# Performance work log

Measured on AMD Instinct MI355X. Metric: run time of the kernel, lower is better.

## Reference

```python
import jax, jax.numpy as jnp
import numpy as np
from jax import lax

K_NEIGHBORS = 15
LAM = 1.0
EPS = 1e-8


def _cdist(a):
    # Euclidean pairwise distance, safe sqrt (zero diag has zero grad path handled in bwd module too)
    sq = jnp.sum(a * a, axis=1)
    d2 = sq[:, None] + sq[None, :] - 2.0 * (a @ a.T)
    d2 = jnp.maximum(d2, 0.0)
    safe = jnp.where(d2 > 0.0, d2, 1.0)
    return jnp.where(d2 > 0.0, jnp.sqrt(safe), 0.0)


def _knn_loss(z, x, k):
    B = x.shape[0]
    x_dist = _cdist(x)
    z_dist = _cdist(z)
    eye = jnp.eye(B, dtype=bool)
    x_ns = jnp.where(eye, jnp.inf, x_dist)  # fill_diagonal_(inf)
    _, knn_idx = lax.top_k(-x_ns, k)        # k smallest per row
    mask = jnp.zeros((B, B), dtype=bool).at[jnp.arange(B)[:, None], knn_idx].set(True)
    mask = mask | mask.T
    x_max = jnp.max(jnp.where(mask, x_dist, -jnp.inf))
    z_max = jnp.max(jnp.where(mask, z_dist, -jnp.inf))
    x_norm = x_dist / (x_max + EPS)
    z_norm = z_dist / (z_max + EPS)
    diff2 = (z_norm - x_norm) ** 2
    # mean over masked entries == masked_select(...).mean()
    return jnp.sum(jnp.where(mask, diff2, 0.0)) / jnp.sum(mask).astype(diff2.dtype)


def setup_inputs() -> dict:
    key = jax.random.key(0)
    ks = jax.random.split(key, 13)
    D, H1, H2, L = 1024, 2048, 512, 64

    def lin(k, fan_in, fan_out):
        bound = 1.0 / np.sqrt(fan_in)
        kw, kb = jax.random.split(k)
        w = jax.random.uniform(kw, (fan_in, fan_out), jnp.float32, -bound, bound)
        b = jax.random.uniform(kb, (fan_out,), jnp.float32, -bound, bound)
        return w, b

    x = jax.random.normal(ks[0], (8192, D), jnp.float32)
    w_e0, b_e0 = lin(ks[1], D, H1)
    w_e1, b_e1 = lin(ks[2], H1, H2)
    w_e2, b_e2 = lin(ks[3], H2, L)
    w_d0, b_d0 = lin(ks[4], L, H2)
    w_d1, b_d1 = lin(ks[5], H2, H1)
    w_d2, b_d2 = lin(ks[6], H1, D)
    return {"x": x,
            "w_e0": w_e0, "b_e0": b_e0, "w_e1": w_e1, "b_e1": b_e1, "w_e2": w_e2, "b_e2": b_e2,
            "w_d0": w_d0, "b_d0": b_d0, "w_d1": w_d1, "b_d1": b_d1, "w_d2": w_d2, "b_d2": b_d2}


def reference(x, w_e0, b_e0, w_e1, b_e1, w_e2, b_e2, w_d0, b_d0, w_d1, b_d1, w_d2, b_d2):
    h = jax.nn.relu(x @ w_e0 + b_e0)
    h = jax.nn.relu(h @ w_e1 + b_e1)
    z = h @ w_e2 + b_e2
    h = jax.nn.relu(z @ w_d0 + b_d0)
    h = jax.nn.relu(h @ w_d1 + b_d1)
    x_rec = h @ w_d2 + b_d2
    rec_loss = jnp.mean((x_rec - x) ** 2)
    knn_loss = _knn_loss(z, x, K_NEIGHBORS)
    total = rec_loss + LAM * knn_loss
    return (total, z, rec_loss, knn_loss)
```

## Files before the change

### kernel.cpp

```cpp
#include <hip/hip_runtime.h>


typedef __attribute__((ext_vector_type(8))) short bf16x8;
typedef __attribute__((ext_vector_type(4))) float f32x4;

#define DEVINL static __device__ __forceinline__

DEVINL unsigned short f2bf(float f){
  unsigned u = __float_as_uint(f);
  u += 0x7FFFu + ((u >> 16) & 1u);
  return (unsigned short)(u >> 16);
}

DEVINL int med3i(int a, int b, int c){
  int d;
  asm("v_med3_i32 %0, %1, %2, %3" : "=v"(d) : "v"(a), "v"(b), "v"(c));
  return d;
}

DEVINL void gload16(const unsigned short* g, void* lds){
  __builtin_amdgcn_global_load_lds(
      (const __attribute__((address_space(1))) unsigned int*)g,
      (__attribute__((address_space(3))) unsigned int*)lds, 16, 0, 0);
}

DEVINL void lds_barrier(){
  asm volatile("s_waitcnt lgkmcnt(0)" ::: "memory");
  __builtin_amdgcn_s_barrier();
  asm volatile("" ::: "memory");
}

#define NLISTS 47

__global__ __launch_bounds__(256) void cvt_rowsq_k(const float* __restrict__ x,
    unsigned short* __restrict__ xb, float* __restrict__ xsq){
  const int lane = threadIdx.x & 63, wv = threadIdx.x >> 6;
  const int row = blockIdx.x * 4 + wv;
  const float4* px = (const float4*)(x + (size_t)row * 1024);
  ushort4* pb = (ushort4*)(xb + (size_t)row * 1024);
  float ss = 0.f;
  #pragma unroll
  for (int q = 0; q < 4; q++){
    float4 v = px[q * 64 + lane];
    ss += v.x*v.x + v.y*v.y + v.z*v.z + v.w*v.w;
    ushort4 o; o.x = f2bf(v.x); o.y = f2bf(v.y); o.z = f2bf(v.z); o.w = f2bf(v.w);
    pb[q * 64 + lane] = o;
  }
  #pragma unroll
  for (int o = 32; o; o >>= 1) ss += __shfl_xor(ss, o);
  if (!lane) xsq[row] = ss;
}

template<int BM, int BN, int WM, int WN, bool RELU, int OMODE>
__global__ __launch_bounds__(256, 2) void gemm_bt(
    const unsigned short* __restrict__ A, const unsigned short* __restrict__ Bt,
    const float* __restrict__ bias, int M, int N, int K,
    unsigned short* __restrict__ Cb, float* __restrict__ Cf,
    const float* __restrict__ Xref, float* __restrict__ recPart)
{
  constexpr int FM = BM / (WM * 16), FN = BN / (WN * 16);
  __shared__ short As[BM][32];
  __shared__ short Bs[BN][32];
  __shared__ float wsum[4];
  const int tid = threadIdx.x, lane = tid & 63, wid = tid >> 6;
  const int wr = wid / WN, wc = wid % WN;
  const int r16 = lane & 15, kg = lane >> 4;
  const int row0 = blockIdx.x * BM, col0 = blockIdx.y * BN;
  const int srow = lane >> 2, scol = (lane & 3) * 8;
  (void)M;
  f32x4 acc[FM][FN] = {};
  for (int k0 = 0; k0 < K; k0 += 32){
    __syncthreads();
    for (int ch = wid; ch < BM/16; ch += 4)
      gload16(A + (size_t)(row0 + ch*16 + srow) * K + k0 + scol, &As[ch*16][0]);
    for (int ch = wid; ch < BN/16; ch += 4)
      gload16(Bt + (size_t)(col0 + ch*16 + srow) * K + k0 + scol, &Bs[ch*16][0]);
    __syncthreads();
    bf16x8 af[FM], bfr[FN];
    #pragma unroll
    for (int m = 0; m < FM; m++) af[m]  = *(const bf16x8*)&As[wr*FM*16 + m*16 + r16][kg*8];
    #pragma unroll
    for (int n = 0; n < FN; n++) bfr[n] = *(const bf16x8*)&Bs[wc*FN*16 + n*16 + r16][kg*8];
    #pragma unroll
    for (int m = 0; m < FM; m++)
      #pragma unroll
      for (int n = 0; n < FN; n++)
        acc[m][n] = __builtin_amdgcn_mfma_f32_16x16x32_bf16(af[m], bfr[n], acc[m][n], 0, 0, 0);
  }
  float lsum = 0.f;
  #pragma unroll
  for (int m = 0; m < FM; m++){
    #pragma unroll
    for (int n = 0; n < FN; n++){
      const int gc = col0 + wc*FN*16 + n*16 + r16;
      const float bv = bias[gc];
      #pragma unroll
      for (int r = 0; r < 4; r++){
        const int gr = row0 + wr*FM*16 + m*16 + kg*4 + r;
        float v = acc[m][n][r] + bv;
        if (RELU) v = fmaxf(v, 0.f);
        if (OMODE == 2){
          float d = v - Xref[(size_t)gr * N + gc];
          lsum += d * d;
        } else {
          Cb[(size_t)gr * N + gc] = f2bf(v);
          if (OMODE == 1) Cf[(size_t)gr * N + gc] = v;
        }
      }
    }
  }
  if (OMODE == 2){
    #pragma unroll
    for (int o = 32; o; o >>= 1) lsum += __shfl_xor(lsum, o);
    if (!lane) wsum[wid] = lsum;
    __syncthreads();
    if (!tid) recPart[blockIdx.y * gridDim.x + blockIdx.x] =
        wsum[0] + wsum[1] + wsum[2] + wsum[3];
  }
}

__global__ __launch_bounds__(256, 2) void gram_topk_k(
    const unsigned short* __restrict__ Xb, const float* __restrict__ xsq,
    int* __restrict__ topP,
    const float* __restrict__ w0, const float* __restrict__ w1,
    const float* __restrict__ w2, const float* __restrict__ w3,
    const float* __restrict__ w4, const float* __restrict__ w5,
    unsigned short* __restrict__ t0, unsigned short* __restrict__ t1,
    unsigned short* __restrict__ t2, unsigned short* __restrict__ t3,
    unsigned short* __restrict__ t4, unsigned short* __restrict__ t5)
{
  __shared__ short As[128][32];
  __shared__ short Bs[128][32];
  __shared__ unsigned short d2s[128][130];
  __shared__ int colL[128][15];
  const int tid = threadIdx.x, lane = tid & 63, wid = tid >> 6;

  if (blockIdx.x >= 512){
    int id = blockIdx.x - 512;
    const float* w; unsigned short* wt; int K, N, loc;
    if      (id < 2048){ w = w0; wt = t0; K = 1024; N = 2048; loc = id; }
    else if (id < 3072){ w = w1; wt = t1; K = 2048; N = 512;  loc = id - 2048; }
    else if (id < 3104){ w = w2; wt = t2; K = 512;  N = 64;   loc = id - 3072; }
    else if (id < 3136){ w = w3; wt = t3; K = 64;   N = 512;  loc = id - 3104; }
    else if (id < 4160){ w = w4; wt = t4; K = 512;  N = 2048; loc = id - 3136; }
    else               { w = w5; wt = t5; K = 2048; N = 1024; loc = id - 4160; }
    const int ntn = N >> 5;
    const int n0 = (loc % ntn) << 5, k0 = (loc / ntn) << 5;
    float (*t)[33] = (float (*)[33])As;
    const int tx = tid & 31, ty = tid >> 5;
    #pragma unroll
    for (int q = 0; q < 4; q++)
      t[ty + 8*q][tx] = w[(size_t)(k0 + ty + 8*q) * N + n0 + tx];
    __syncthreads();
    #pragma unroll
    for (int q = 0; q < 4; q++)
      wt[(size_t)(n0 + ty + 8*q) * K + k0 + tx] = f2bf(t[tx][ty + 8*q]);
    return;
  }

  const int wr = wid >> 1, wc = wid & 1;
  const int r16 = lane & 15, kg = lane >> 4;
  const int srow = lane >> 2, scol = (lane & 3) * 8;
  const float INF = __builtin_inff();
  const int INFI = 0x7FFFFFFF;

  const int bi = blockIdx.x & 63;
  const int cl = blockIdx.x >> 6;
  const int row0 = bi * 128;
  const int ntt = (cl == 7) ? 5 : 4;

  const int selrow = tid & 127, half = tid >> 7, selc0 = half * 64;

  auto stage = [&](int j0s, int k0s){
    for (int ch = wid; ch < 8; ch += 4){
      gload16(Xb + (size_t)(row0 + ch*16 + srow) * 1024 + k0s + scol, &As[ch*16][0]);
      gload16(Xb + (size_t)(j0s  + ch*16 + srow) * 1024 + k0s + scol, &Bs[ch*16][0]);
    }
  };

  int r0,r1,r2,r3,r4,r5,r6,r7,r8,r9,r10,r11,r12,r13,r14;
  r0=r1=r2=r3=r4=r5=r6=r7=r8=r9=r10=r11=r12=r13=r14=INFI;
  auto insR = [&](int v){
    if (v < r14){
      r14 = med3i(v, r13, r14); r13 = med3i(v, r12, r13);
      r12 = med3i(v, r11, r12); r11 = med3i(v, r10, r11);
      r10 = med3i(v, r9 , r10); r9  = med3i(v, r8 , r9 );
      r8  = med3i(v, r7 , r8 ); r7  = med3i(v, r6 , r7 );
      r6  = med3i(v, r5 , r6 ); r5  = med3i(v, r4 , r5 );
      r4  = med3i(v, r3 , r4 ); r3  = med3i(v, r2 , r3 );
      r2  = med3i(v, r1 , r2 ); r1  = med3i(v, r0 , r1 );
      r0  = min(r0, v);
    }
  };
  int c0,c1,c2,c3,c4,c5,c6,c7,c8,c9,c10,c11,c12,c13,c14;
  auto insC = [&](int v){
    if (v < c14){
      c14 = med3i(v, c13, c14); c13 = med3i(v, c12, c13);
      c12 = med3i(v, c11, c12); c11 = med3i(v, c10, c11);
      c10 = med3i(v, c9 , c10); c9  = med3i(v, c8 , c9 );
      c8  = med3i(v, c7 , c8 ); c7  = med3i(v, c6 , c7 );
      c6  = med3i(v, c5 , c6 ); c5  = med3i(v, c4 , c5 );
      c4  = med3i(v, c3 , c4 ); c3  = med3i(v, c2 , c3 );
      c2  = med3i(v, c1 , c2 ); c1  = med3i(v, c0 , c1 );
      c0  = min(c0, v);
    }
  };

  float xr[4][4];
  #pragma unroll
  for (int m = 0; m < 4; m++)
    #pragma unroll
    for (int r = 0; r < 4; r++)
      xr[m][r] = xsq[row0 + wr*64 + m*16 + kg*4 + r];

  stage(((bi + cl * 4) & 63) * 128, 0);

  for (int tt = 0; tt < ntt; ++tt){
    const int d = cl * 4 + tt;
    const int bj = (bi + d) & 63;
    const int j0 = bj * 128;
    f32x4 acc[4][4] = {};
    for (int k0 = 0; k0 < 1024; k0 += 32){
      __syncthreads();
      bf16x8 af[4], bfr[4];
      #pragma unroll
      for (int m = 0; m < 4; m++) af[m]  = *(const bf16x8*)&As[wr*64 + m*16 + r16][kg*8];
      #pragma unroll
      for (int n = 0; n < 4; n++) bfr[n] = *(const bf16x8*)&Bs[wc*64 + n*16 + r16][kg*8];
      __syncthreads();
      if (k0 + 32 < 1024)      stage(j0, k0 + 32);
      else if (tt + 1 < ntt)   stage(((bi + d + 1) & 63) * 128, 0);
      #pragma unroll
      for (int m = 0; m < 4; m++)
        #pragma unroll
        for (int n = 0; n < 4; n++)
          acc[m][n] = __builtin_amdgcn_mfma_f32_16x16x32_bf16(af[m], bfr[n], acc[m][n], 0, 0, 0);
    }
    float xc[4];
    #pragma unroll
    for (int n = 0; n < 4; n++) xc[n] = xsq[j0 + wc*64 + n*16 + r16];
    #pragma unroll
    for (int m = 0; m < 4; m++){
      #pragma unroll
      for (int n = 0; n < 4; n++){
        const int lc = wc*64 + n*16 + r16;
        #pragma unroll
        for (int r = 0; r < 4; r++){
          const int lr = wr*64 + m*16 + kg*4 + r;
          float v = xr[m][r] + xc[n] - 2.f * acc[m][n][r];
          if (row0 + lr == j0 + lc) v = INF;
          d2s[lr][lc] = f2bf(v);
        }
      }
    }
    lds_barrier();
    const int jg0 = j0 + selc0;
    #pragma unroll 4
    for (int cc = 0; cc < 64; cc += 2){
      unsigned pv = *(const unsigned*)&d2s[selrow][selc0 + cc];
      insR((int)(((pv & 0xFFFFu) << 16) | (unsigned)(jg0 + cc)));
      insR((int)((pv & 0xFFFF0000u) | (unsigned)(jg0 + cc + 1)));
    }
    const bool doCol = (d >= 1) && (d <= 31);
    if (doCol){
      c0=c1=c2=c3=c4=c5=c6=c7=c8=c9=c10=c11=c12=c13=c14=INFI;
      const int rbase = row0 + selc0;
      #pragma unroll 4
      for (int rr = 0; rr < 64; ++rr){
        unsigned v = d2s[selc0 + rr][selrow];
        insC((int)((v << 16) | (unsigned)(rbase + rr)));
      }
      if (half){
        colL[selrow][0]=c0;  colL[selrow][1]=c1;  colL[selrow][2]=c2;
        colL[selrow][3]=c3;  colL[selrow][4]=c4;  colL[selrow][5]=c5;
        colL[selrow][6]=c6;  colL[selrow][7]=c7;  colL[selrow][8]=c8;
        colL[selrow][9]=c9;  colL[selrow][10]=c10; colL[selrow][11]=c11;
        colL[selrow][12]=c12; colL[selrow][13]=c13; colL[selrow][14]=c14;
      }
    }
    lds_barrier();
    if (doCol && !half){
      #pragma unroll 1
      for (int q = 0; q < 15; ++q){
        int v = colL[selrow][q];
        if (v >= c14) break;
        insC(v);
      }
      int* dst = topP + ((size_t)(j0 + selrow) * NLISTS + (16 + d - 1)) * 15;
      dst[0]=c0;  dst[1]=c1;  dst[2]=c2;  dst[3]=c3;  dst[4]=c4;
      dst[5]=c5;  dst[6]=c6;  dst[7]=c7;  dst[8]=c8;  dst[9]=c9;
      dst[10]=c10; dst[11]=c11; dst[12]=c12; dst[13]=c13; dst[14]=c14;
    }
  }
  int* dst = topP + ((size_t)(row0 + selrow) * NLISTS + (2 * cl + half)) * 15;
  dst[0]=r0;  dst[1]=r1;  dst[2]=r2;  dst[3]=r3;  dst[4]=r4;
  dst[5]=r5;  dst[6]=r6;  dst[7]=r7;  dst[8]=r8;  dst[9]=r9;
  dst[10]=r10; dst[11]=r11; dst[12]=r12; dst[13]=r13; dst[14]=r14;
}

__global__ __launch_bounds__(256) void merge_topk_k(const int* __restrict__ topP,
    int* __restrict__ knn, float* __restrict__ d2k, float* __restrict__ xpart)
{
  __shared__ float wmax[4];
  const int lane = threadIdx.x & 63, wid = threadIdx.x >> 6;
  const int row = blockIdx.x * 4 + wid;
  const int* tp = topP + (size_t)row * (NLISTS * 15);
  const int INFI = 0x7FFFFFFF;
  int c0  = tp[lane];
  int c1  = tp[lane + 64];
  int c2  = tp[lane + 128];
  int c3  = tp[lane + 192];
  int c4  = tp[lane + 256];
  int c5  = tp[lane + 320];
  int c6  = tp[lane + 384];
  int c7  = tp[lane + 448];
  int c8  = tp[lane + 512];
  int c9  = tp[lane + 576];
  int c10 = tp[lane + 640];
  int c11 = (lane + 704 < 705) ? tp[lane + 704] : INFI;
  float last = 0.f;
  for (int it = 0; it < 15; ++it){
    int m = min(min(min(c0, c1), min(c2, c3)), min(min(c4, c5), min(c6, c7)));
    m = min(m, min(min(c8, c9), min(c10, c11)));
    #pragma unroll
    for (int o = 32; o; o >>= 1) m = min(m, __shfl_xor(m, o));
    if (!lane){
      knn[row * 15 + it] = m & 0xFFFF;
      float f = __uint_as_float((unsigned)m & 0xFFFF0000u);
      d2k[row * 15 + it] = f;
      last = f;
    }
    c0  = (c0  == m) ? INFI : c0;   c1  = (c1  == m) ? INFI : c1;
    c2  = (c2  == m) ? INFI : c2;   c3  = (c3  == m) ? INFI : c3;
    c4  = (c4  == m) ? INFI : c4;   c5  = (c5  == m) ? INFI : c5;
    c6  = (c6  == m) ? INFI : c6;   c7  = (c7  == m) ? INFI : c7;
    c8  = (c8  == m) ? INFI : c8;   c9  = (c9  == m) ? INFI : c9;
    c10 = (c10 == m) ? INFI : c10;  c11 = (c11 == m) ? INFI : c11;
  }
  if (!lane) wmax[wid] = last;
  __syncthreads();
  if (!threadIdx.x)
    xpart[blockIdx.x] = fmaxf(fmaxf(wmax[0], wmax[1]), fmaxf(wmax[2], wmax[3]));
}

__global__ void mask_build_k(const int* __restrict__ knn, unsigned* __restrict__ mask){
  int t = blockIdx.x * blockDim.x + threadIdx.x;
  if (t >= 8192 * 15) return;
  int i = t / 15, j = knn[t];
  atomicOr(&mask[i * 256 + (j >> 5)], 1u << (j & 31));
  atomicOr(&mask[j * 256 + (i >> 5)], 1u << (i & 31));
}

__global__ __launch_bounds__(256) void rowcnt_k(const unsigned* __restrict__ mask,
                                                int* __restrict__ rowcnt){
  const int lane = threadIdx.x & 63, wid = threadIdx.x >> 6;
  const int row = blockIdx.x * 4 + wid;
  const unsigned* mr = mask + (size_t)row * 256;
  int pc = __popc(mr[lane]) + __popc(mr[64+lane]) + __popc(mr[128+lane]) + __popc(mr[192+lane]);
  #pragma unroll
  for (int o = 32; o; o >>= 1) pc += __shfl_xor(pc, o);
  if (!lane) rowcnt[row] = pc;
}

__global__ __launch_bounds__(1024) void scan_k(const int* __restrict__ rowcnt,
                                               int* __restrict__ rowbase, int* __restrict__ count){
  __shared__ int sc[1024];
  const int t = threadIdx.x;
  int local[8];
  int s = 0;
  #pragma unroll
  for (int q = 0; q < 8; q++){ local[q] = s; s += rowcnt[t * 8 + q]; }
  sc[t] = s;
  __syncthreads();
  for (int o = 1; o < 1024; o <<= 1){
    int v = (t >= o) ? sc[t - o] : 0;
    __syncthreads();
    sc[t] += v;
    __syncthreads();
  }
  const int base = t ? sc[t - 1] : 0;
  #pragma unroll
  for (int q = 0; q < 8; q++) rowbase[t * 8 + q] = base + local[q];
  if (t == 1023) count[0] = sc[1023];
}

__global__ __launch_bounds__(256) void gather2_k(const unsigned* __restrict__ mask,
                                                 const int* __restrict__ rowbase,
                                                 unsigned* __restrict__ pairs){
  const int lane = threadIdx.x & 63, wid = threadIdx.x >> 6;
  const int row = blockIdx.x * 4 + wid;
  const unsigned* mr = mask + (size_t)row * 256;
  unsigned w0 = mr[lane], w1 = mr[64+lane], w2 = mr[128+lane], w3 = mr[192+lane];
  const int pc = __popc(w0) + __popc(w1) + __popc(w2) + __popc(w3);
  int s = pc;
  for (int o = 1; o < 64; o <<= 1){
    int v = __shfl_up(s, o);
    if (lane >= o) s += v;
  }
  int base = rowbase[row] + s - pc;
  const unsigned hi = (unsigned)row << 16;
  unsigned w; int jb;
  w = w0; jb = lane * 32;
  while (w){ int b = __ffs(w) - 1; w &= w - 1; pairs[base++] = hi | (unsigned)(jb + b); }
  w = w1; jb = (64 + lane) * 32;
  while (w){ int b = __ffs(w) - 1; w &= w - 1; pairs[base++] = hi | (unsigned)(jb + b); }
  w = w2; jb = (128 + lane) * 32;
  while (w){ int b = __ffs(w) - 1; w &= w - 1; pairs[base++] = hi | (unsigned)(jb + b); }
  w = w3; jb = (192 + lane) * 32;
  while (w){ int b = __ffs(w) - 1; w &= w - 1; pairs[base++] = hi | (unsigned)(jb + b); }
}

__global__ __launch_bounds__(256) void pair_sums_k(
    const unsigned* __restrict__ pairs, const int* __restrict__ count,
    const float* __restrict__ z, const int* __restrict__ knn, const float* __restrict__ d2k,
    float* __restrict__ zzP, float* __restrict__ zxP, float* __restrict__ xxP,
    float* __restrict__ zmP)
{
  __shared__ float red[4][4];
  const int lane = threadIdx.x & 63, wid = threadIdx.x >> 6;
  const int n = *count;
  float szz = 0.f, szx = 0.f, sxx = 0.f, mz = 0.f;
  for (int p = blockIdx.x * 4 + wid; p < n; p += gridDim.x * 4){
    const unsigned pr = pairs[p];
    const int i = (int)(pr >> 16), j = (int)(pr & 0xFFFFu);
    float d = z[i * 64 + lane] - z[j * 64 + lane];
    float s = d * d;
    #pragma unroll
    for (int o = 32; o; o >>= 1) s += __shfl_xor(s, o);
    int ki = knn[i * 15 + min(lane, 14)];
    unsigned long long m1 = __ballot(lane < 15 && ki == j);
    float dx2;
    if (m1){
      dx2 = d2k[i * 15 + (__ffsll(m1) - 1)];
    } else {
      int kj = knn[j * 15 + min(lane, 14)];
      unsigned long long m2 = __ballot(lane < 15 && kj == i);
      dx2 = d2k[j * 15 + (__ffsll(m2) - 1)];
    }
    float dz = sqrtf(s), dx = sqrtf(dx2);
    szz += s;
    szx += dz * dx;
    sxx += dx2;
    mz = fmaxf(mz, dz);
  }
  if (!lane){ red[wid][0] = szz; red[wid][1] = szx; red[wid][2] = sxx; red[wid][3] = mz; }
  __syncthreads();
  if (!threadIdx.x){
    float a = 0.f, b = 0.f, c = 0.f, m = 0.f;
    #pragma unroll
    for (int w = 0; w < 4; w++){
      a += red[w][0]; b += red[w][1]; c += red[w][2]; m = fmaxf(m, red[w][3]);
    }
    zzP[blockIdx.x] = a; zxP[blockIdx.x] = b; xxP[blockIdx.x] = c; zmP[blockIdx.x] = m;
  }
}

__global__ __launch_bounds__(256) void final_reduce_k(
    const float* __restrict__ recPart, const float* __restrict__ xpart,
    const float* __restrict__ zzP, const float* __restrict__ zxP,
    const float* __restrict__ xxP, const float* __restrict__ zmP,
    const int* __restrict__ count, float* __restrict__ out)
{
  __shared__ float rd[4][6];
  const int t = threadIdx.x, lane = t & 63, wid = t >> 6;
  float rec = 0.f, xm = 0.f, zz = 0.f, zx = 0.f, xx = 0.f, zm = 0.f;
  for (int i = t; i < 1024; i += 256) rec += recPart[i];
  for (int i = t; i < 2048; i += 256) xm = fmaxf(xm, xpart[i]);
  for (int i = t; i < 1920; i += 256){
    zz += zzP[i]; zx += zxP[i]; xx += xxP[i]; zm = fmaxf(zm, zmP[i]);
  }
  #pragma unroll
  for (int o = 32; o; o >>= 1){
    rec += __shfl_xor(rec, o); zz += __shfl_xor(zz, o);
    zx  += __shfl_xor(zx, o);  xx += __shfl_xor(xx, o);
    xm = fmaxf(xm, __shfl_xor(xm, o));
    zm = fmaxf(zm, __shfl_xor(zm, o));
  }
  if (!lane){
    rd[wid][0]=rec; rd[wid][1]=zz; rd[wid][2]=zx; rd[wid][3]=xx; rd[wid][4]=xm; rd[wid][5]=zm;
  }
  __syncthreads();
  if (!t){
    rec = rd[0][0]+rd[1][0]+rd[2][0]+rd[3][0];
    zz  = rd[0][1]+rd[1][1]+rd[2][1]+rd[3][1];
    zx  = rd[0][2]+rd[1][2]+rd[2][2]+rd[3][2];
    xx  = rd[0][3]+rd[1][3]+rd[2][3]+rd[3][3];
    xm  = fmaxf(fmaxf(rd[0][4],rd[1][4]), fmaxf(rd[2][4],rd[3][4]));
    zm  = fmaxf(fmaxf(rd[0][5],rd[1][5]), fmaxf(rd[2][5],rd[3][5]));
    rec *= 1.0f / (8192.0f * 1024.0f);
    float xmax = sqrtf(xm);
    float rx = 1.0f / (xmax + 1e-8f), rz = 1.0f / (zm + 1e-8f);
    float knn = (zz * rz * rz - 2.0f * zx * rz * rx + xx * rx * rx) / (float)count[0];
    out[0] = rec + knn;
    out[1 + 8192 * 64]     = rec;
    out[1 + 8192 * 64 + 1] = knn;
  }
}

extern "C" void kernel_launch(void* const* d_in, const int* in_sizes, int n_in,
                              void* d_out, int out_size, void* d_ws, size_t ws_size,
                              hipStream_t stream)
{
  (void)in_sizes; (void)n_in; (void)out_size;
  const float* x    = (const float*)d_in[0];
  const float* w_e0 = (const float*)d_in[1];  const float* b_e0 = (const float*)d_in[2];
  const float* w_e1 = (const float*)d_in[3];  const float* b_e1 = (const float*)d_in[4];
  const float* w_e2 = (const float*)d_in[5];  const float* b_e2 = (const float*)d_in[6];
  const float* w_d0 = (const float*)d_in[7];  const float* b_d0 = (const float*)d_in[8];
  const float* w_d1 = (const float*)d_in[9];  const float* b_d1 = (const float*)d_in[10];
  const float* w_d2 = (const float*)d_in[11]; const float* b_d2 = (const float*)d_in[12];
  float* out = (float*)d_out;

  char* ws = (char*)d_ws;
  size_t off = 0;
  auto alloc = [&](size_t bytes) -> void* {
    void* p = ws + off;
    off += (bytes + 255) & ~(size_t)255;
    return p;
  };
  unsigned short* xb   = (unsigned short*)alloc(8192ull * 1024 * 2);
  unsigned short* wte0 = (unsigned short*)alloc(2048ull * 1024 * 2);
  unsigned short* wte1 = (unsigned short*)alloc(512ull  * 2048 * 2);
  unsigned short* wte2 = (unsigned short*)alloc(64ull   * 512  * 2);
  unsigned short* wtd0 = (unsigned short*)alloc(512ull  * 64   * 2);
  unsigned short* wtd1 = (unsigned short*)alloc(2048ull * 512  * 2);
  unsigned short* wtd2 = (unsigned short*)alloc(1024ull * 2048 * 2);
  unsigned short* bufA = (unsigned short*)alloc(8192ull * 2048 * 2);
  unsigned short* bufB = (unsigned short*)alloc(8192ull * 512  * 2);
  unsigned short* zb   = (unsigned short*)alloc(8192ull * 64   * 2);
  float* xsq    = (float*)alloc(8192 * 4);
  int*   knn    = (int*)  alloc(8192ull * 15 * 4);
  float* d2k    = (float*)alloc(8192ull * 15 * 4);
  unsigned* mask = (unsigned*)alloc(8192ull * 256 * 4);
  int*   rowcnt = (int*)  alloc(8192 * 4);
  int*   rowbase= (int*)  alloc(8192 * 4);
  unsigned* pairs = (unsigned*)alloc(245760ull * 4);
  float* xpart  = (float*)alloc(2048 * 4);
  float* zzP    = (float*)alloc(1920 * 4);
  float* zxP    = (float*)alloc(1920 * 4);
  float* xxP    = (float*)alloc(1920 * 4);
  float* zmP    = (float*)alloc(1920 * 4);
  float* recPart= (float*)alloc(1024 * 4);
  int*   count  = (int*)  alloc(256);
  if (off > ws_size) return;

  int* topP = (int*)bufA;

  hipMemsetAsync(mask, 0, 8192ull * 256 * 4, stream);

  cvt_rowsq_k<<<2048, 256, 0, stream>>>(x, xb, xsq);

  gram_topk_k<<<6720, 256, 0, stream>>>(xb, xsq, topP,
      w_e0, w_e1, w_e2, w_d0, w_d1, w_d2, wte0, wte1, wte2, wtd0, wtd1, wtd2);
  merge_topk_k<<<2048, 256, 0, stream>>>(topP, knn, d2k, xpart);
  mask_build_k<<<(8192 * 15 + 255) / 256, 256, 0, stream>>>(knn, mask);
  rowcnt_k<<<2048, 256, 0, stream>>>(mask, rowcnt);
  scan_k<<<1, 1024, 0, stream>>>(rowcnt, rowbase, count);
  gather2_k<<<2048, 256, 0, stream>>>(mask, rowbase, pairs);

  gemm_bt<128,128,2,2,true ,0><<<dim3(64,16), 256, 0, stream>>>(xb,   wte0, b_e0, 8192, 2048, 1024, bufA, nullptr, nullptr, nullptr);
  gemm_bt<128, 64,2,2,true ,0><<<dim3(64, 8), 256, 0, stream>>>(bufA, wte1, b_e1, 8192,  512, 2048, bufB, nullptr, nullptr, nullptr);
  gemm_bt< 32, 64,2,2,false,1><<<dim3(256,1), 256, 0, stream>>>(bufB, wte2, b_e2, 8192,   64,  512, zb,   out + 1, nullptr, nullptr);
  gemm_bt<128, 64,2,2,true ,0><<<dim3(64, 8), 256, 0, stream>>>(zb,   wtd0, b_d0, 8192,  512,   64, bufB, nullptr, nullptr, nullptr);
  gemm_bt<128,128,2,2,true ,0><<<dim3(64,16), 256, 0, stream>>>(bufB, wtd1, b_d1, 8192, 2048,  512, bufA, nullptr, nullptr, nullptr);
  gemm_bt< 64,128,2,2,false,2><<<dim3(128,8), 256, 0, stream>>>(bufA, wtd2, b_d2, 8192, 1024, 2048, nullptr, nullptr, x, recPart);

  pair_sums_k<<<1920, 256, 0, stream>>>(pairs, count, out + 1, knn, d2k, zzP, zxP, xxP, zmP);
  final_reduce_k<<<1, 256, 0, stream>>>(recPart, xpart, zzP, zxP, xxP, zmP, count, out);
}
```

Baseline: 434.3 us.

## Prefilter kNN candidates with diagonal-block threshold, drop mask pipeline, fuse layer-0 GEMM

Adds a pass that computes a per-row 15th-smallest distance bound from each row's own 128-row diagonal block. The gram/top-k kernel uses this bound to reject most candidates before the med3 insertion network, buffering survivors in LDS, and merges the two half-row lists in-block so fewer partial lists are written. The weight transpose moves into the conversion kernel, and the first encoder GEMM runs as extra blocks inside the gram kernel so the two overlap. The bitmask build, row count, scan and gather kernels are replaced by iterating over kNN pairs directly, weighting each pair by whether it is mutual. This cuts launch count and global traffic, but adds the threshold kernel and puts a heavier mix of work into one kernel.

```diff
diff --git a/kernel.cpp b/kernel.cpp
--- a/kernel.cpp
+++ b/kernel.cpp
@@ -30,11 +30,55 @@
   asm volatile("" ::: "memory");
 }
 
-#define NLISTS 47
-
-__global__ __launch_bounds__(256) void cvt_rowsq_k(const float* __restrict__ x,
-    unsigned short* __restrict__ xb, float* __restrict__ xsq){
-  const int lane = threadIdx.x & 63, wv = threadIdx.x >> 6;
+#define NLISTS 39
+
+#define INS15(NAME, R0,R1,R2,R3,R4,R5,R6,R7,R8,R9,R10,R11,R12,R13,R14)  \
+  auto NAME = [&](int v){                                               \
+    if (v < R14){                                                       \
+      R14 = med3i(v, R13, R14); R13 = med3i(v, R12, R13);               \
+      R12 = med3i(v, R11, R12); R11 = med3i(v, R10, R11);               \
+      R10 = med3i(v, R9 , R10); R9  = med3i(v, R8 , R9 );               \
+      R8  = med3i(v, R7 , R8 ); R7  = med3i(v, R6 , R7 );               \
+      R6  = med3i(v, R5 , R6 ); R5  = med3i(v, R4 , R5 );               \
+      R4  = med3i(v, R3 , R4 ); R3  = med3i(v, R2 , R3 );               \
+      R2  = med3i(v, R1 , R2 ); R1  = med3i(v, R0 , R1 );               \
+      R0  = min(R0, v);                                                 \
+    }                                                                   \
+  }
+
+__global__ __launch_bounds__(256) void cvtT_k(const float* __restrict__ x,
+    unsigned short* __restrict__ xb, float* __restrict__ xsq,
+    const float* __restrict__ w0, const float* __restrict__ w1,
+    const float* __restrict__ w2, const float* __restrict__ w3,
+    const float* __restrict__ w4, const float* __restrict__ w5,
+    unsigned short* __restrict__ t0, unsigned short* __restrict__ t1,
+    unsigned short* __restrict__ t2, unsigned short* __restrict__ t3,
+    unsigned short* __restrict__ t4, unsigned short* __restrict__ t5)
+{
+  __shared__ float t[32][33];
+  const int tid = threadIdx.x;
+  if (blockIdx.x >= 2048){
+    int id = blockIdx.x - 2048;
+    const float* w; unsigned short* wt; int K, N, loc;
+    if      (id < 2048){ w = w0; wt = t0; K = 1024; N = 2048; loc = id; }
+    else if (id < 3072){ w = w1; wt = t1; K = 2048; N = 512;  loc = id - 2048; }
+    else if (id < 3104){ w = w2; wt = t2; K = 512;  N = 64;   loc = id - 3072; }
+    else if (id < 3136){ w = w3; wt = t3; K = 64;   N = 512;  loc = id - 3104; }
+    else if (id < 4160){ w = w4; wt = t4; K = 512;  N = 2048; loc = id - 3136; }
+    else               { w = w5; wt = t5; K = 2048; N = 1024; loc = id - 4160; }
+    const int ntn = N >> 5;
+    const int n0 = (loc % ntn) << 5, k0 = (loc / ntn) << 5;
+    const int tx = tid & 31, ty = tid >> 5;
+    #pragma unroll
+    for (int q = 0; q < 4; q++)
+      t[ty + 8*q][tx] = w[(size_t)(k0 + ty + 8*q) * N + n0 + tx];
+    __syncthreads();
+    #pragma unroll
+    for (int q = 0; q < 4; q++)
+      wt[(size_t)(n0 + ty + 8*q) * K + k0 + tx] = f2bf(t[tx][ty + 8*q]);
+    return;
+  }
+  const int lane = tid & 63, wv = tid >> 6;
   const int row = blockIdx.x * 4 + wv;
   const float4* px = (const float4*)(x + (size_t)row * 1024);
   ushort4* pb = (ushort4*)(xb + (size_t)row * 1024);
@@ -49,6 +93,75 @@
   #pragma unroll
   for (int o = 32; o; o >>= 1) ss += __shfl_xor(ss, o);
   if (!lane) xsq[row] = ss;
+}
+
+__global__ __launch_bounds__(256, 2) void thr_k(
+    const unsigned short* __restrict__ Xb, const float* __restrict__ xsq,
+    int* __restrict__ thrI)
+{
+  __shared__ short As[128][32];
+  __shared__ unsigned short d2s[128][130];
+  const int tid = threadIdx.x, lane = tid & 63, wid = tid >> 6;
+  const int wr = wid >> 1, wc = wid & 1;
+  const int r16 = lane & 15, kg = lane >> 4;
+  const int srow = lane >> 2, scol = (lane & 3) * 8;
+  const float INF = __builtin_inff();
+  const int b0 = blockIdx.x * 128;
+
+  float xr[4][4];
+  #pragma unroll
+  for (int m = 0; m < 4; m++)
+    #pragma unroll
+    for (int r = 0; r < 4; r++)
+      xr[m][r] = xsq[b0 + wr*64 + m*16 + kg*4 + r];
+
+  f32x4 acc[4][4] = {};
+  for (int k0 = 0; k0 < 1024; k0 += 32){
+    __syncthreads();
+    for (int ch = wid; ch < 8; ch += 4)
+      gload16(Xb + (size_t)(b0 + ch*16 + srow) * 1024 + k0 + scol, &As[ch*16][0]);
+    __syncthreads();
+    bf16x8 af[4], bfr[4];
+    #pragma unroll
+    for (int m = 0; m < 4; m++) af[m]  = *(const bf16x8*)&As[wr*64 + m*16 + r16][kg*8];
+    #pragma unroll
+    for (int n = 0; n < 4; n++) bfr[n] = *(const bf16x8*)&As[wc*64 + n*16 + r16][kg*8];
+    #pragma unroll
+    for (int m = 0; m < 4; m++)
+      #pragma unroll
+      for (int n = 0; n < 4; n++)
+        acc[m][n] = __builtin_amdgcn_mfma_f32_16x16x32_bf16(af[m], bfr[n], acc[m][n], 0, 0, 0);
+  }
+  float xc[4];
+  #pragma unroll
+  for (int n = 0; n < 4; n++) xc[n] = xsq[b0 + wc*64 + n*16 + r16];
+  #pragma unroll
+  for (int m = 0; m < 4; m++){
+    #pragma unroll
+    for (int n = 0; n < 4; n++){
+      const int lc = wc*64 + n*16 + r16;
+      #pragma unroll
+      for (int r = 0; r < 4; r++){
+        const int lr = wr*64 + m*16 + kg*4 + r;
+        float v = xr[m][r] + xc[n] - 2.f * acc[m][n][r];
+        if (lr == lc) v = INF;
+        d2s[lr][lc] = f2bf(v);
+      }
+    }
+  }
+  __syncthreads();
+  if (tid < 128){
+    int r0,r1,r2,r3,r4,r5,r6,r7,r8,r9,r10,r11,r12,r13,r14;
+    r0=r1=r2=r3=r4=r5=r6=r7=r8=r9=r10=r11=r12=r13=r14=0x7FFFFFFF;
+    INS15(ins, r0,r1,r2,r3,r4,r5,r6,r7,r8,r9,r10,r11,r12,r13,r14);
+    #pragma unroll 4
+    for (int cc = 0; cc < 128; cc += 2){
+      unsigned pv = *(const unsigned*)&d2s[tid][cc];
+      ins((int)((pv << 16) | (unsigned)cc));
+      ins((int)((pv & 0xFFFF0000u) | (unsigned)(cc + 1)));
+    }
+    thrI[b0 + tid] = (int)(((unsigned)r14 & 0xFFFF0000u) | 0xFFFFu);
+  }
 }
 
 template<int BM, int BN, int WM, int WN, bool RELU, int OMODE>
@@ -121,55 +234,66 @@
 
 __global__ __launch_bounds__(256, 2) void gram_topk_k(
     const unsigned short* __restrict__ Xb, const float* __restrict__ xsq,
-    int* __restrict__ topP,
-    const float* __restrict__ w0, const float* __restrict__ w1,
-    const float* __restrict__ w2, const float* __restrict__ w3,
-    const float* __restrict__ w4, const float* __restrict__ w5,
-    unsigned short* __restrict__ t0, unsigned short* __restrict__ t1,
-    unsigned short* __restrict__ t2, unsigned short* __restrict__ t3,
-    unsigned short* __restrict__ t4, unsigned short* __restrict__ t5)
+    const int* __restrict__ thrI, int* __restrict__ topP,
+    const unsigned short* __restrict__ gBt, const float* __restrict__ gBias,
+    unsigned short* __restrict__ gC)
 {
   __shared__ short As[128][32];
   __shared__ short Bs[128][32];
   __shared__ unsigned short d2s[128][130];
   __shared__ int colL[128][15];
+  __shared__ unsigned bkt[16][256];
   const int tid = threadIdx.x, lane = tid & 63, wid = tid >> 6;
-
-  if (blockIdx.x >= 512){
-    int id = blockIdx.x - 512;
-    const float* w; unsigned short* wt; int K, N, loc;
-    if      (id < 2048){ w = w0; wt = t0; K = 1024; N = 2048; loc = id; }
-    else if (id < 3072){ w = w1; wt = t1; K = 2048; N = 512;  loc = id - 2048; }
-    else if (id < 3104){ w = w2; wt = t2; K = 512;  N = 64;   loc = id - 3072; }
-    else if (id < 3136){ w = w3; wt = t3; K = 64;   N = 512;  loc = id - 3104; }
-    else if (id < 4160){ w = w4; wt = t4; K = 512;  N = 2048; loc = id - 3136; }
-    else               { w = w5; wt = t5; K = 2048; N = 1024; loc = id - 4160; }
-    const int ntn = N >> 5;
-    const int n0 = (loc % ntn) << 5, k0 = (loc / ntn) << 5;
-    float (*t)[33] = (float (*)[33])As;
-    const int tx = tid & 31, ty = tid >> 5;
-    #pragma unroll
-    for (int q = 0; q < 4; q++)
-      t[ty + 8*q][tx] = w[(size_t)(k0 + ty + 8*q) * N + n0 + tx];
-    __syncthreads();
-    #pragma unroll
-    for (int q = 0; q < 4; q++)
-      wt[(size_t)(n0 + ty + 8*q) * K + k0 + tx] = f2bf(t[tx][ty + 8*q]);
-    return;
-  }
-
   const int wr = wid >> 1, wc = wid & 1;
   const int r16 = lane & 15, kg = lane >> 4;
   const int srow = lane >> 2, scol = (lane & 3) * 8;
+
+  if (blockIdx.x >= 512){
+    const int gb = blockIdx.x - 512;
+    const int row0 = (gb & 63) * 128, col0 = (gb >> 6) * 128;
+    f32x4 acc[4][4] = {};
+    for (int k0 = 0; k0 < 1024; k0 += 32){
+      __syncthreads();
+      for (int ch = wid; ch < 8; ch += 4){
+        gload16(Xb  + (size_t)(row0 + ch*16 + srow) * 1024 + k0 + scol, &As[ch*16][0]);
+        gload16(gBt + (size_t)(col0 + ch*16 + srow) * 1024 + k0 + scol, &Bs[ch*16][0]);
+      }
+      __syncthreads();
+      bf16x8 af[4], bfr[4];
+      #pragma unroll
+      for (int m = 0; m < 4; m++) af[m]  = *(const bf16x8*)&As[wr*64 + m*16 + r16][kg*8];
+      #pragma unroll
+      for (int n = 0; n < 4; n++) bfr[n] = *(const bf16x8*)&Bs[wc*64 + n*16 + r16][kg*8];
+      #pragma unroll
+      for (int m = 0; m < 4; m++)
+        #pragma unroll
+        for (int n = 0; n < 4; n++)
+          acc[m][n] = __builtin_amdgcn_mfma_f32_16x16x32_bf16(af[m], bfr[n], acc[m][n], 0, 0, 0);
+    }
+    #pragma unroll
+    for (int m = 0; m < 4; m++){
+      #pragma unroll
+      for (int n = 0; n < 4; n++){
+        const int gc = col0 + wc*64 + n*16 + r16;
+        const float bv = gBias[gc];
+        #pragma unroll
+        for (int r = 0; r < 4; r++){
+          const int gr = row0 + wr*64 + m*16 + kg*4 + r;
+          gC[(size_t)gr * 2048 + gc] = f2bf(fmaxf(acc[m][n][r] + bv, 0.f));
+        }
+      }
+    }
+    return;
+  }
+
   const float INF = __builtin_inff();
   const int INFI = 0x7FFFFFFF;
-
   const int bi = blockIdx.x & 63;
   const int cl = blockIdx.x >> 6;
   const int row0 = bi * 128;
   const int ntt = (cl == 7) ? 5 : 4;
-
   const int selrow = tid & 127, half = tid >> 7, selc0 = half * 64;
+  const int thrRI = thrI[row0 + selrow];
 
   auto stage = [&](int j0s, int k0s){
     for (int ch = wid; ch < 8; ch += 4){
@@ -180,31 +304,9 @@
 
   int r0,r1,r2,r3,r4,r5,r6,r7,r8,r9,r10,r11,r12,r13,r14;
   r0=r1=r2=r3=r4=r5=r6=r7=r8=r9=r10=r11=r12=r13=r14=INFI;
-  auto insR = [&](int v){
-    if (v < r14){
-      r14 = med3i(v, r13, r14); r13 = med3i(v, r12, r13);
-      r12 = med3i(v, r11, r12); r11 = med3i(v, r10, r11);
-      r10 = med3i(v, r9 , r10); r9  = med3i(v, r8 , r9 );
-      r8  = med3i(v, r7 , r8 ); r7  = med3i(v, r6 , r7 );
-      r6  = med3i(v, r5 , r6 ); r5  = med3i(v, r4 , r5 );
-      r4  = med3i(v, r3 , r4 ); r3  = med3i(v, r2 , r3 );
-      r2  = med3i(v, r1 , r2 ); r1  = med3i(v, r0 , r1 );
-      r0  = min(r0, v);
-    }
-  };
+  INS15(insR, r0,r1,r2,r3,r4,r5,r6,r7,r8,r9,r10,r11,r12,r13,r14);
   int c0,c1,c2,c3,c4,c5,c6,c7,c8,c9,c10,c11,c12,c13,c14;
-  auto insC = [&](int v){
-    if (v < c14){
-      c14 = med3i(v, c13, c14); c13 = med3i(v, c12, c13);
-      c12 = med3i(v, c11, c12); c11 = med3i(v, c10, c11);
-      c10 = med3i(v, c9 , c10); c9  = med3i(v, c8 , c9 );
-      c8  = med3i(v, c7 , c8 ); c7  = med3i(v, c6 , c7 );
-      c6  = med3i(v, c5 , c6 ); c5  = med3i(v, c4 , c5 );
-      c4  = med3i(v, c3 , c4 ); c3  = med3i(v, c2 , c3 );
-      c2  = med3i(v, c1 , c2 ); c1  = med3i(v, c0 , c1 );
-      c0  = min(c0, v);
-    }
-  };
+  INS15(insC, c0,c1,c2,c3,c4,c5,c6,c7,c8,c9,c10,c11,c12,c13,c14);
 
   float xr[4][4];
   #pragma unroll
@@ -254,22 +356,40 @@
       }
     }
     lds_barrier();
-    const int jg0 = j0 + selc0;
-    #pragma unroll 4
-    for (int cc = 0; cc < 64; cc += 2){
-      unsigned pv = *(const unsigned*)&d2s[selrow][selc0 + cc];
-      insR((int)(((pv & 0xFFFFu) << 16) | (unsigned)(jg0 + cc)));
-      insR((int)((pv & 0xFFFF0000u) | (unsigned)(jg0 + cc + 1)));
-    }
+
+    {
+      int cnt = 0;
+      const int jg0 = j0 + selc0;
+      #pragma unroll 4
+      for (int cc = 0; cc < 64; cc += 2){
+        unsigned pv = *(const unsigned*)&d2s[selrow][selc0 + cc];
+        int p0 = (int)((pv << 16) | (unsigned)(jg0 + cc));
+        int p1 = (int)((pv & 0xFFFF0000u) | (unsigned)(jg0 + cc + 1));
+        if (p0 <= thrRI){
+          if (cnt < 16){ bkt[cnt][tid] = (unsigned)p0; ++cnt; } else insR(p0);
+        }
+        if (p1 <= thrRI){
+          if (cnt < 16){ bkt[cnt][tid] = (unsigned)p1; ++cnt; } else insR(p1);
+        }
+      }
+      for (int q = 0; q < cnt; ++q) insR((int)bkt[q][tid]);
+    }
+
     const bool doCol = (d >= 1) && (d <= 31);
     if (doCol){
       c0=c1=c2=c3=c4=c5=c6=c7=c8=c9=c10=c11=c12=c13=c14=INFI;
+      const int thrCI = thrI[j0 + selrow];
       const int rbase = row0 + selc0;
+      int cnt = 0;
       #pragma unroll 4
       for (int rr = 0; rr < 64; ++rr){
         unsigned v = d2s[selc0 + rr][selrow];
-        insC((int)((v << 16) | (unsigned)(rbase + rr)));
-      }
+        int pk = (int)((v << 16) | (unsigned)(rbase + rr));
+        if (pk <= thrCI){
+          if (cnt < 16){ bkt[cnt][tid] = (unsigned)pk; ++cnt; } else insC(pk);
+        }
+      }
+      for (int q = 0; q < cnt; ++q) insC((int)bkt[q][tid]);
       if (half){
         colL[selrow][0]=c0;  colL[selrow][1]=c1;  colL[selrow][2]=c2;
         colL[selrow][3]=c3;  colL[selrow][4]=c4;  colL[selrow][5]=c5;
@@ -286,16 +406,33 @@
         if (v >= c14) break;
         insC(v);
       }
-      int* dst = topP + ((size_t)(j0 + selrow) * NLISTS + (16 + d - 1)) * 15;
+      int* dst = topP + ((size_t)(j0 + selrow) * NLISTS + (8 + d - 1)) * 15;
       dst[0]=c0;  dst[1]=c1;  dst[2]=c2;  dst[3]=c3;  dst[4]=c4;
       dst[5]=c5;  dst[6]=c6;  dst[7]=c7;  dst[8]=c8;  dst[9]=c9;
       dst[10]=c10; dst[11]=c11; dst[12]=c12; dst[13]=c13; dst[14]=c14;
     }
   }
-  int* dst = topP + ((size_t)(row0 + selrow) * NLISTS + (2 * cl + half)) * 15;
-  dst[0]=r0;  dst[1]=r1;  dst[2]=r2;  dst[3]=r3;  dst[4]=r4;
-  dst[5]=r5;  dst[6]=r6;  dst[7]=r7;  dst[8]=r8;  dst[9]=r9;
-  dst[10]=r10; dst[11]=r11; dst[12]=r12; dst[13]=r13; dst[14]=r14;
+  lds_barrier();
+  if (half){
+    colL[selrow][0]=r0;  colL[selrow][1]=r1;  colL[selrow][2]=r2;
+    colL[selrow][3]=r3;  colL[selrow][4]=r4;  colL[selrow][5]=r5;
+    colL[selrow][6]=r6;  colL[selrow][7]=r7;  colL[selrow][8]=r8;
+    colL[selrow][9]=r9;  colL[selrow][10]=r10; colL[selrow][11]=r11;
+    colL[selrow][12]=r12; colL[selrow][13]=r13; colL[selrow][14]=r14;
+  }
+  lds_barrier();
+  if (!half){
+    #pragma unroll 1
+    for (int q = 0; q < 15; ++q){
+      int v = colL[selrow][q];
+      if (v >= r14) break;
+      insR(v);
+    }
+    int* dst = topP + ((size_t)(row0 + selrow) * NLISTS + cl) * 15;
+    dst[0]=r0;  dst[1]=r1;  dst[2]=r2;  dst[3]=r3;  dst[4]=r4;
+    dst[5]=r5;  dst[6]=r6;  dst[7]=r7;  dst[8]=r8;  dst[9]=r9;
+    dst[10]=r10; dst[11]=r11; dst[12]=r12; dst[13]=r13; dst[14]=r14;
+  }
 }
 
 __global__ __launch_bounds__(256) void merge_topk_k(const int* __restrict__ topP,
@@ -306,22 +443,20 @@
   const int row = blockIdx.x * 4 + wid;
   const int* tp = topP + (size_t)row * (NLISTS * 15);
   const int INFI = 0x7FFFFFFF;
-  int c0  = tp[lane];
-  int c1  = tp[lane + 64];
-  int c2  = tp[lane + 128];
-  int c3  = tp[lane + 192];
-  int c4  = tp[lane + 256];
-  int c5  = tp[lane + 320];
-  int c6  = tp[lane + 384];
-  int c7  = tp[lane + 448];
-  int c8  = tp[lane + 512];
-  int c9  = tp[lane + 576];
-  int c10 = tp[lane + 640];
-  int c11 = (lane + 704 < 705) ? tp[lane + 704] : INFI;
+  int c0 = tp[lane];
+  int c1 = tp[lane + 64];
+  int c2 = tp[lane + 128];
+  int c3 = tp[lane + 192];
+  int c4 = tp[lane + 256];
+  int c5 = tp[lane + 320];
+  int c6 = tp[lane + 384];
+  int c7 = tp[lane + 448];
+  int c8 = tp[lane + 512];
+  int c9 = (lane < 9) ? tp[lane + 576] : INFI;
   float last = 0.f;
   for (int it = 0; it < 15; ++it){
     int m = min(min(min(c0, c1), min(c2, c3)), min(min(c4, c5), min(c6, c7)));
-    m = min(m, min(min(c8, c9), min(c10, c11)));
+    m = min(m, min(c8, c9));
     #pragma unroll
     for (int o = 32; o; o >>= 1) m = min(m, __shfl_xor(m, o));
     if (!lane){
@@ -330,12 +465,11 @@
       d2k[row * 15 + it] = f;
       last = f;
     }
-    c0  = (c0  == m) ? INFI : c0;   c1  = (c1  == m) ? INFI : c1;
-    c2  = (c2  == m) ? INFI : c2;   c3  = (c3  == m) ? INFI : c3;
-    c4  = (c4  == m) ? INFI : c4;   c5  = (c5  == m) ? INFI : c5;
-    c6  = (c6  == m) ? INFI : c6;   c7  = (c7  == m) ? INFI : c7;
-    c8  = (c8  == m) ? INFI : c8;   c9  = (c9  == m) ? INFI : c9;
-    c10 = (c10 == m) ? INFI : c10;  c11 = (c11 == m) ? INFI : c11;
+    c0 = (c0 == m) ? INFI : c0;   c1 = (c1 == m) ? INFI : c1;
+    c2 = (c2 == m) ? INFI : c2;   c3 = (c3 == m) ? INFI : c3;
+    c4 = (c4 == m) ? INFI : c4;   c5 = (c5 == m) ? INFI : c5;
+    c6 = (c6 == m) ? INFI : c6;   c7 = (c7 == m) ? INFI : c7;
+    c8 = (c8 == m) ? INFI : c8;   c9 = (c9 == m) ? INFI : c9;
   }
   if (!lane) wmax[wid] = last;
   __syncthreads();
@@ -343,115 +477,47 @@
     xpart[blockIdx.x] = fmaxf(fmaxf(wmax[0], wmax[1]), fmaxf(wmax[2], wmax[3]));
 }
 
-__global__ void mask_build_k(const int* __restrict__ knn, unsigned* __restrict__ mask){
-  int t = blockIdx.x * blockDim.x + threadIdx.x;
-  if (t >= 8192 * 15) return;
-  int i = t / 15, j = knn[t];
-  atomicOr(&mask[i * 256 + (j >> 5)], 1u << (j & 31));
-  atomicOr(&mask[j * 256 + (i >> 5)], 1u << (i & 31));
-}
-
-__global__ __launch_bounds__(256) void rowcnt_k(const unsigned* __restrict__ mask,
-                                                int* __restrict__ rowcnt){
+__global__ __launch_bounds__(256) void pair_sums_k(
+    const float* __restrict__ z, const int* __restrict__ knn,
+    const float* __restrict__ d2k,
+    float* __restrict__ zzP, float* __restrict__ zxP, float* __restrict__ xxP,
+    float* __restrict__ zmP, float* __restrict__ cntP)
+{
+  __shared__ float red[4][5];
   const int lane = threadIdx.x & 63, wid = threadIdx.x >> 6;
-  const int row = blockIdx.x * 4 + wid;
-  const unsigned* mr = mask + (size_t)row * 256;
-  int pc = __popc(mr[lane]) + __popc(mr[64+lane]) + __popc(mr[128+lane]) + __popc(mr[192+lane]);
-  #pragma unroll
-  for (int o = 32; o; o >>= 1) pc += __shfl_xor(pc, o);
-  if (!lane) rowcnt[row] = pc;
-}
-
-__global__ __launch_bounds__(1024) void scan_k(const int* __restrict__ rowcnt,
-                                               int* __restrict__ rowbase, int* __restrict__ count){
-  __shared__ int sc[1024];
-  const int t = threadIdx.x;
-  int local[8];
-  int s = 0;
-  #pragma unroll
-  for (int q = 0; q < 8; q++){ local[q] = s; s += rowcnt[t * 8 + q]; }
-  sc[t] = s;
-  __syncthreads();
-  for (int o = 1; o < 1024; o <<= 1){
-    int v = (t >= o) ? sc[t - o] : 0;
-    __syncthreads();
-    sc[t] += v;
-    __syncthreads();
-  }
-  const int base = t ? sc[t - 1] : 0;
-  #pragma unroll
-  for (int q = 0; q < 8; q++) rowbase[t * 8 + q] = base + local[q];
-  if (t == 1023) count[0] = sc[1023];
-}
-
-__global__ __launch_bounds__(256) void gather2_k(const unsigned* __restrict__ mask,
-                                                 const int* __restrict__ rowbase,
-                                                 unsigned* __restrict__ pairs){
-  const int lane = threadIdx.x & 63, wid = threadIdx.x >> 6;
-  const int row = blockIdx.x * 4 + wid;
-  const unsigned* mr = mask + (size_t)row * 256;
-  unsigned w0 = mr[lane], w1 = mr[64+lane], w2 = mr[128+lane], w3 = mr[192+lane];
-  const int pc = __popc(w0) + __popc(w1) + __popc(w2) + __popc(w3);
-  int s = pc;
-  for (int o = 1; o < 64; o <<= 1){
-    int v = __shfl_up(s, o);
-    if (lane >= o) s += v;
-  }
-  int base = rowbase[row] + s - pc;
-  const unsigned hi = (unsigned)row << 16;
-  unsigned w; int jb;
-  w = w0; jb = lane * 32;
-  while (w){ int b = __ffs(w) - 1; w &= w - 1; pairs[base++] = hi | (unsigned)(jb + b); }
-  w = w1; jb = (64 + lane) * 32;
-  while (w){ int b = __ffs(w) - 1; w &= w - 1; pairs[base++] = hi | (unsigned)(jb + b); }
-  w = w2; jb = (128 + lane) * 32;
-  while (w){ int b = __ffs(w) - 1; w &= w - 1; pairs[base++] = hi | (unsigned)(jb + b); }
-  w = w3; jb = (192 + lane) * 32;
-  while (w){ int b = __ffs(w) - 1; w &= w - 1; pairs[base++] = hi | (unsigned)(jb + b); }
-}
-
-__global__ __launch_bounds__(256) void pair_sums_k(
-    const unsigned* __restrict__ pairs, const int* __restrict__ count,
-    const float* __restrict__ z, const int* __restrict__ knn, const float* __restrict__ d2k,
-    float* __restrict__ zzP, float* __restrict__ zxP, float* __restrict__ xxP,
-    float* __restrict__ zmP)
-{
-  __shared__ float red[4][4];
-  const int lane = threadIdx.x & 63, wid = threadIdx.x >> 6;
-  const int n = *count;
-  float szz = 0.f, szx = 0.f, sxx = 0.f, mz = 0.f;
-  for (int p = blockIdx.x * 4 + wid; p < n; p += gridDim.x * 4){
-    const unsigned pr = pairs[p];
-    const int i = (int)(pr >> 16), j = (int)(pr & 0xFFFFu);
-    float d = z[i * 64 + lane] - z[j * 64 + lane];
-    float s = d * d;
+  float szz = 0.f, szx = 0.f, sxx = 0.f, mz = 0.f, scnt = 0.f;
+  for (int p = blockIdx.x * 4 + wid; p < 122880; p += gridDim.x * 4){
+    const int i = p / 15;
+    const int j = knn[p];
+    const float dx2 = d2k[p];
+    float dd = z[(size_t)i * 64 + lane] - z[(size_t)j * 64 + lane];
+    float s = dd * dd;
     #pragma unroll
     for (int o = 32; o; o >>= 1) s += __shfl_xor(s, o);
-    int ki = knn[i * 15 + min(lane, 14)];
-    unsigned long long m1 = __ballot(lane < 15 && ki == j);
-    float dx2;
-    if (m1){
-      dx2 = d2k[i * 15 + (__ffsll(m1) - 1)];
-    } else {
-      int kj = knn[j * 15 + min(lane, 14)];
-      unsigned long long m2 = __ballot(lane < 15 && kj == i);
-      dx2 = d2k[j * 15 + (__ffsll(m2) - 1)];
-    }
+    int kj = knn[j * 15 + min(lane, 14)];
+    unsigned long long m2 = __ballot(lane < 15 && kj == i);
+    const float w = m2 ? 1.f : 2.f;
     float dz = sqrtf(s), dx = sqrtf(dx2);
-    szz += s;
-    szx += dz * dx;
-    sxx += dx2;
+    szz += w * s;
+    szx += w * dz * dx;
+    sxx += w * dx2;
+    scnt += w;
     mz = fmaxf(mz, dz);
   }
-  if (!lane){ red[wid][0] = szz; red[wid][1] = szx; red[wid][2] = sxx; red[wid][3] = mz; }
+  if (!lane){
+    red[wid][0] = szz; red[wid][1] = szx; red[wid][2] = sxx;
+    red[wid][3] = mz;  red[wid][4] = scnt;
+  }
   __syncthreads();
   if (!threadIdx.x){
-    float a = 0.f, b = 0.f, c = 0.f, m = 0.f;
+    float a = 0.f, b = 0.f, c = 0.f, m = 0.f, n = 0.f;
     #pragma unroll
     for (int w = 0; w < 4; w++){
-      a += red[w][0]; b += red[w][1]; c += red[w][2]; m = fmaxf(m, red[w][3]);
-    }
-    zzP[blockIdx.x] = a; zxP[blockIdx.x] = b; xxP[blockIdx.x] = c; zmP[blockIdx.x] = m;
+      a += red[w][0]; b += red[w][1]; c += red[w][2];
+      m = fmaxf(m, red[w][3]); n += red[w][4];
+    }
+    zzP[blockIdx.x] = a; zxP[blockIdx.x] = b; xxP[blockIdx.x] = c;
+    zmP[blockIdx.x] = m; cntP[blockIdx.x] = n;
   }
 }
 
@@ -459,25 +525,28 @@
     const float* __restrict__ recPart, const float* __restrict__ xpart,
     const float* __restrict__ zzP, const float* __restrict__ zxP,
     const float* __restrict__ xxP, const float* __restrict__ zmP,
-    const int* __restrict__ count, float* __restrict__ out)
-{
-  __shared__ float rd[4][6];
+    const float* __restrict__ cntP, float* __restrict__ out)
+{
+  __shared__ float rd[4][7];
   const int t = threadIdx.x, lane = t & 63, wid = t >> 6;
-  float rec = 0.f, xm = 0.f, zz = 0.f, zx = 0.f, xx = 0.f, zm = 0.f;
+  float rec = 0.f, xm = 0.f, zz = 0.f, zx = 0.f, xx = 0.f, zm = 0.f, cnt = 0.f;
   for (int i = t; i < 1024; i += 256) rec += recPart[i];
   for (int i = t; i < 2048; i += 256) xm = fmaxf(xm, xpart[i]);
   for (int i = t; i < 1920; i += 256){
-    zz += zzP[i]; zx += zxP[i]; xx += xxP[i]; zm = fmaxf(zm, zmP[i]);
+    zz += zzP[i]; zx += zxP[i]; xx += xxP[i]; cnt += cntP[i];
+    zm = fmaxf(zm, zmP[i]);
   }
   #pragma unroll
   for (int o = 32; o; o >>= 1){
     rec += __shfl_xor(rec, o); zz += __shfl_xor(zz, o);
     zx  += __shfl_xor(zx, o);  xx += __shfl_xor(xx, o);
+    cnt += __shfl_xor(cnt, o);
     xm = fmaxf(xm, __shfl_xor(xm, o));
     zm = fmaxf(zm, __shfl_xor(zm, o));
   }
   if (!lane){
-    rd[wid][0]=rec; rd[wid][1]=zz; rd[wid][2]=zx; rd[wid][3]=xx; rd[wid][4]=xm; rd[wid][5]=zm;
+    rd[wid][0]=rec; rd[wid][1]=zz; rd[wid][2]=zx; rd[wid][3]=xx;
+    rd[wid][4]=xm;  rd[wid][5]=zm; rd[wid][6]=cnt;
   }
   __syncthreads();
   if (!t){
@@ -487,10 +556,11 @@
     xx  = rd[0][3]+rd[1][3]+rd[2][3]+rd[3][3];
     xm  = fmaxf(fmaxf(rd[0][4],rd[1][4]), fmaxf(rd[2][4],rd[3][4]));
     zm  = fmaxf(fmaxf(rd[0][5],rd[1][5]), fmaxf(rd[2][5],rd[3][5]));
+    cnt = rd[0][6]+rd[1][6]+rd[2][6]+rd[3][6];
     rec *= 1.0f / (8192.0f * 1024.0f);
     float xmax = sqrtf(xm);
     float rx = 1.0f / (xmax + 1e-8f), rz = 1.0f / (zm + 1e-8f);
-    float knn = (zz * rz * rz - 2.0f * zx * rz * rx + xx * rx * rx) / (float)count[0];
+    float knn = (zz * rz * rz - 2.0f * zx * rz * rx + xx * rx * rx) / cnt;
     out[0] = rec + knn;
     out[1 + 8192 * 64]     = rec;
     out[1 + 8192 * 64 + 1] = knn;
@@ -528,43 +598,34 @@
   unsigned short* bufA = (unsigned short*)alloc(8192ull * 2048 * 2);
   unsigned short* bufB = (unsigned short*)alloc(8192ull * 512  * 2);
   unsigned short* zb   = (unsigned short*)alloc(8192ull * 64   * 2);
+  int*   topP   = (int*)  alloc(8192ull * NLISTS * 15 * 4);
   float* xsq    = (float*)alloc(8192 * 4);
+  int*   thrI   = (int*)  alloc(8192 * 4);
   int*   knn    = (int*)  alloc(8192ull * 15 * 4);
   float* d2k    = (float*)alloc(8192ull * 15 * 4);
-  unsigned* mask = (unsigned*)alloc(8192ull * 256 * 4);
-  int*   rowcnt = (int*)  alloc(8192 * 4);
-  int*   rowbase= (int*)  alloc(8192 * 4);
-  unsigned* pairs = (unsigned*)alloc(245760ull * 4);
   float* xpart  = (float*)alloc(2048 * 4);
   float* zzP    = (float*)alloc(1920 * 4);
   float* zxP    = (float*)alloc(1920 * 4);
   float* xxP    = (float*)alloc(1920 * 4);
   float* zmP    = (float*)alloc(1920 * 4);
+  float* cntP   = (float*)alloc(1920 * 4);
   float* recPart= (float*)alloc(1024 * 4);
-  int*   count  = (int*)  alloc(256);
   if (off > ws_size) return;
 
-  int* topP = (int*)bufA;
-
-  hipMemsetAsync(mask, 0, 8192ull * 256 * 4, stream);
-
-  cvt_rowsq_k<<<2048, 256, 0, stream>>>(x, xb, xsq);
-
-  gram_topk_k<<<6720, 256, 0, stream>>>(xb, xsq, topP,
+  cvtT_k<<<8256, 256, 0, stream>>>(x, xb, xsq,
       w_e0, w_e1, w_e2, w_d0, w_d1, w_d2, wte0, wte1, wte2, wtd0, wtd1, wtd2);
+
+  thr_k<<<64, 256, 0, stream>>>(xb, xsq, thrI);
+
+  gram_topk_k<<<1536, 256, 0, stream>>>(xb, xsq, thrI, topP, wte0, b_e0, bufA);
   merge_topk_k<<<2048, 256, 0, stream>>>(topP, knn, d2k, xpart);
-  mask_build_k<<<(8192 * 15 + 255) / 256, 256, 0, stream>>>(knn, mask);
-  rowcnt_k<<<2048, 256, 0, stream>>>(mask, rowcnt);
-  scan_k<<<1, 1024, 0, stream>>>(rowcnt, rowbase, count);
-  gather2_k<<<2048, 256, 0, stream>>>(mask, rowbase, pairs);
-
-  gemm_bt<128,128,2,2,true ,0><<<dim3(64,16), 256, 0, stream>>>(xb,   wte0, b_e0, 8192, 2048, 1024, bufA, nullptr, nullptr, nullptr);
+
   gemm_bt<128, 64,2,2,true ,0><<<dim3(64, 8), 256, 0, stream>>>(bufA, wte1, b_e1, 8192,  512, 2048, bufB, nullptr, nullptr, nullptr);
   gemm_bt< 32, 64,2,2,false,1><<<dim3(256,1), 256, 0, stream>>>(bufB, wte2, b_e2, 8192,   64,  512, zb,   out + 1, nullptr, nullptr);
   gemm_bt<128, 64,2,2,true ,0><<<dim3(64, 8), 256, 0, stream>>>(zb,   wtd0, b_d0, 8192,  512,   64, bufB, nullptr, nullptr, nullptr);
   gemm_bt<128,128,2,2,true ,0><<<dim3(64,16), 256, 0, stream>>>(bufB, wtd1, b_d1, 8192, 2048,  512, bufA, nullptr, nullptr, nullptr);
   gemm_bt< 64,128,2,2,false,2><<<dim3(128,8), 256, 0, stream>>>(bufA, wtd2, b_d2, 8192, 1024, 2048, nullptr, nullptr, x, recPart);
 
-  pair_sums_k<<<1920, 256, 0, stream>>>(pairs, count, out + 1, knn, d2k, zzP, zxP, xxP, zmP);
-  final_reduce_k<<<1, 256, 0, stream>>>(recPart, xpart, zzP, zxP, xxP, zmP, count, out);
-}
+  pair_sums_k<<<1920, 256, 0, stream>>>(out + 1, knn, d2k, zzP, zxP, xxP, zmP, cntP);
+  final_reduce_k<<<1, 256, 0, stream>>>(recPart, xpart, zzP, zxP, xxP, zmP, cntP, out);
+}
```

New measurement: 418.7 us. -3.6%, faster.
